# Performance work log

Hardware: AMD Instinct MI355X
Metric: run time of the kernel (lower is better)

The kernel has to match this reference:

```python
import jax, jax.numpy as jnp
import numpy as np

B, S, HID = 1, 2048, 4096
N_HEADS, N_KV_HEADS = 32, 8
HEAD_DIM = HID // N_HEADS  # 128


def setup_inputs() -> dict:
    key = jax.random.key(0)
    ks = jax.random.split(key, 5)
    w = 0.02  # init scale for weights
    return {
        "hidden_states": jax.random.normal(ks[0], (B, S, HID), dtype=jnp.float32),
        "Wq": jax.random.normal(ks[1], (HID, HID), dtype=jnp.float32) * w,
        "Wk": jax.random.normal(ks[2], (N_KV_HEADS * HEAD_DIM, HID), dtype=jnp.float32) * w,
        "Wv": jax.random.normal(ks[3], (N_KV_HEADS * HEAD_DIM, HID), dtype=jnp.float32) * w,
        "Wo": jax.random.normal(ks[4], (HID, HID), dtype=jnp.float32) * w,
        "n_init": 4,
        "n_local": 1024,
    }


def reference(hidden_states, Wq, Wk, Wv, Wo, n_init, n_local):
    b, s, hid = hidden_states.shape
    n_rep = N_HEADS // N_KV_HEADS
    scale = 1.0 / np.sqrt(HEAD_DIM).astype(np.float32)

    # QKV projections (torch Linear: y = x @ W.T)
    q = (hidden_states @ Wq.T).reshape(b, s, N_HEADS, HEAD_DIM).transpose(0, 2, 1, 3)
    k = (hidden_states @ Wk.T).reshape(b, s, N_KV_HEADS, HEAD_DIM).transpose(0, 2, 1, 3)
    v = (hidden_states @ Wv.T).reshape(b, s, N_KV_HEADS, HEAD_DIM).transpose(0, 2, 1, 3)

    # GQA: repeat KV heads to match query heads
    k = jnp.repeat(k, n_rep, axis=1)  # [b, H, s, d]
    v = jnp.repeat(v, n_rep, axis=1)

    scores = jnp.einsum('bhqd,bhkd->bhqk', q, k) * scale  # [b, H, s, s]

    # StreamingLLM mask: causal AND (attention sink OR sliding window)
    i = jnp.arange(s)[:, None]
    j = jnp.arange(s)[None, :]
    allowed = (j <= i) & ((j < n_init) | (i - j < n_local))  # [s, s]
    neg = jnp.finfo(scores.dtype).min
    scores = jnp.where(allowed[None, None], scores, neg)

    probs = jax.nn.softmax(scores, axis=-1)
    attn = jnp.einsum('bhqk,bhkd->bhqd', probs, v)  # [b, H, s, d]
    attn = attn.transpose(0, 2, 1, 3).reshape(b, s, hid)
    return attn @ Wo.T
```

## Files before the change

kernel.cpp:

```cpp
#include <hip/hip_runtime.h>
#include <hip/hip_bf16.h>

#define S     2048
#define HID   4096
#define NH    32
#define NKV   8
#define DH    128
#define KVD   1024
#define NQK   6144
#define KDIM  4096

typedef unsigned short ushort_t;
typedef __attribute__((ext_vector_type(8))) __bf16 bf16x8;
typedef __attribute__((ext_vector_type(8))) unsigned short u16x8;
typedef __attribute__((ext_vector_type(4))) float f32x4;

static __device__ __forceinline__ unsigned short f2b(float f) {
    union { float f; unsigned int i; } x; x.f = f;
    unsigned int r = (x.i + 0x7fffu + ((x.i >> 16) & 1u)) >> 16;
    return (unsigned short)r;
}

static __device__ __forceinline__ void gload16(const void* g, void* l) {
    __builtin_amdgcn_global_load_lds(
        (const __attribute__((address_space(1))) void*)g,
        (__attribute__((address_space(3))) void*)l, 16, 0, 0);
}

__global__ __launch_bounds__(256)
void cvt_f2b(const float* __restrict__ src, ushort_t* __restrict__ dst, int n4) {
    int i = blockIdx.x * 256 + threadIdx.x;
    if (i < n4) {
        float4 v = ((const float4*)src)[i];
        ushort4 o;
        o.x = f2b(v.x); o.y = f2b(v.y); o.z = f2b(v.z); o.w = f2b(v.w);
        ((ushort4*)dst)[i] = o;
    }
}

#define G_BM 256
#define G_BN 128
#define G_BK 64
#define BUF_USH ((G_BM + G_BN) * G_BK)
#define BOFF_B  (G_BM * G_BK)

#define STG_A(bb, kt2, j) gload16(gA[j] + (size_t)(kt2) * G_BK, &sm[(bb) + ldA[j]])
#define STG_B(bb, kt2, j) gload16(gB[j] + (size_t)(kt2) * G_BK, &sm[(bb) + ldB[j]])

template <int MODE>
__global__ __launch_bounds__(512, 2)
void gemm256(const ushort_t* __restrict__ A, const ushort_t* __restrict__ B,
             float* __restrict__ Cf, ushort_t* __restrict__ Qb,
             ushort_t* __restrict__ Kb, ushort_t* __restrict__ Vt,
             int M, int N, int K) {
    __shared__ __align__(16) ushort_t sm[3 * BUF_USH];

    const int tid   = threadIdx.x;
    const int w     = tid >> 6;
    const int lane  = tid & 63;
    const int mlane = lane & 15;
    const int q4    = lane >> 4;
    const int wr    = w >> 1, wc = w & 1;
    const int m0    = blockIdx.y * G_BM;
    const int n0    = blockIdx.x * G_BN;

    const ushort_t* gA[4];
    const ushort_t* gB[2];
    int ldA[4], ldB[2];
#pragma unroll
    for (int j = 0; j < 4; j++) {
        int c = j * 512 + tid, row = c >> 3, sl = (c & 7) ^ (row & 7);
        gA[j]  = A + (size_t)(m0 + row) * K + sl * 8;
        ldA[j] = (j * 512 + w * 64) * 8;
    }
#pragma unroll
    for (int j = 0; j < 2; j++) {
        int c = j * 512 + tid, row = c >> 3, sl = (c & 7) ^ (row & 7);
        gB[j]  = B + (size_t)(n0 + row) * K + sl * 8;
        ldB[j] = BOFF_B + (j * 512 + w * 64) * 8;
    }

    int offA[4][2], offB[4][2];
#pragma unroll
    for (int f = 0; f < 4; f++)
#pragma unroll
        for (int ks = 0; ks < 2; ks++) {
            int ra = wr * 64 + f * 16 + mlane;
            offA[f][ks] = ra * 64 + (((ks * 4 + q4) ^ (ra & 7)) * 8);
            int rb = wc * 64 + f * 16 + mlane;
            offB[f][ks] = BOFF_B + rb * 64 + (((ks * 4 + q4) ^ (rb & 7)) * 8);
        }

    f32x4 acc[4][4];
#pragma unroll
    for (int i = 0; i < 4; i++)
#pragma unroll
        for (int j = 0; j < 4; j++) acc[i][j] = (f32x4)(0.0f);

    const int NT = K / G_BK;

    STG_A(0, 0, 0); STG_A(0, 0, 1); STG_A(0, 0, 2); STG_A(0, 0, 3);
    STG_B(0, 0, 0); STG_B(0, 0, 1);
    STG_A(BUF_USH, 1, 0); STG_A(BUF_USH, 1, 1);
    STG_A(BUF_USH, 1, 2); STG_A(BUF_USH, 1, 3);
    STG_B(BUF_USH, 1, 0); STG_B(BUF_USH, 1, 1);
    asm volatile("s_waitcnt vmcnt(6)" ::: "memory");
    __builtin_amdgcn_s_barrier();

    int s_cur = 0;
    for (int kt = 0; kt < NT; kt++) {
        const int s_n2 = (s_cur >= 1) ? s_cur - 1 : 2;
        const int base = s_cur * BUF_USH;
        const int b2   = s_n2 * BUF_USH;
        const bool stg = (kt + 2) < NT;

#pragma unroll
        for (int p = 0; p < 4; p++) {
            const int qm = p >> 1, qn = p & 1;
            bf16x8 af[2][2], bq[2][2];
#pragma unroll
            for (int mi = 0; mi < 2; mi++)
#pragma unroll
                for (int ks = 0; ks < 2; ks++)
                    af[mi][ks] = *(const bf16x8*)&sm[base + offA[qm * 2 + mi][ks]];
#pragma unroll
            for (int ni = 0; ni < 2; ni++)
#pragma unroll
                for (int ks = 0; ks < 2; ks++)
                    bq[ni][ks] = *(const bf16x8*)&sm[base + offB[qn * 2 + ni][ks]];

            if (stg) {
                if (p == 0) { STG_A(b2, kt + 2, 0); STG_A(b2, kt + 2, 1); }
                if (p == 1) { STG_A(b2, kt + 2, 2); STG_A(b2, kt + 2, 3); }
                if (p == 2) { STG_B(b2, kt + 2, 0); }
                if (p == 3) { STG_B(b2, kt + 2, 1); }
            }

            __builtin_amdgcn_s_barrier();
            asm volatile("s_waitcnt lgkmcnt(0)");
            __builtin_amdgcn_s_setprio(1);
#pragma unroll
            for (int mi = 0; mi < 2; mi++)
#pragma unroll
                for (int ni = 0; ni < 2; ni++)
#pragma unroll
                    for (int ks = 0; ks < 2; ks++)
                        acc[qm * 2 + mi][qn * 2 + ni] =
                            __builtin_amdgcn_mfma_f32_16x16x32_bf16(
                                af[mi][ks], bq[ni][ks],
                                acc[qm * 2 + mi][qn * 2 + ni], 0, 0, 0);
            __builtin_amdgcn_s_setprio(0);
            __builtin_amdgcn_s_barrier();
        }

        if (stg) asm volatile("s_waitcnt vmcnt(6)" ::: "memory");
        else     asm volatile("s_waitcnt vmcnt(0)" ::: "memory");
        __builtin_amdgcn_s_barrier();
        s_cur = (s_cur == 2) ? 0 : s_cur + 1;
    }

#pragma unroll
    for (int fm = 0; fm < 4; fm++) {
#pragma unroll
        for (int fn = 0; fn < 4; fn++) {
            const int row = m0 + wr * 64 + fm * 16 + q4 * 4;
            const int col = n0 + wc * 64 + fn * 16 + mlane;
            if (MODE == 0) {
#pragma unroll
                for (int r = 0; r < 4; r++)
                    Cf[(size_t)(row + r) * N + col] = acc[fm][fn][r];
            } else {
                if (n0 < HID) {
#pragma unroll
                    for (int r = 0; r < 4; r++)
                        Qb[(size_t)(row + r) * HID + col] = f2b(acc[fm][fn][r]);
                } else if (n0 < HID + KVD) {
                    int c2 = col - HID;
#pragma unroll
                    for (int r = 0; r < 4; r++)
                        Kb[(size_t)(row + r) * KVD + c2] = f2b(acc[fm][fn][r]);
                } else {
                    int c2 = col - (HID + KVD);
                    ushort4 o;
                    o.x = f2b(acc[fm][fn][0]); o.y = f2b(acc[fm][fn][1]);
                    o.z = f2b(acc[fm][fn][2]); o.w = f2b(acc[fm][fn][3]);
                    *(ushort4*)(Vt + (size_t)c2 * S + row) = o;
                }
            }
        }
    }
}

__global__ __launch_bounds__(256)
void attn_mfma(const ushort_t* __restrict__ Qb, const ushort_t* __restrict__ Kb,
               const ushort_t* __restrict__ Vt, ushort_t* __restrict__ O,
               const int* __restrict__ n_init_p, const int* __restrict__ n_local_p) {
    __shared__ ushort_t Ks[4][32][40];
    __shared__ ushort_t Vs[128][40];
    __shared__ ushort_t Ps[4][16][40];

    const int n_init = *n_init_p, n_local = *n_local_p;
    const int tid   = threadIdx.x;
    const int w     = tid >> 6;
    const int lane  = tid & 63;
    const int mlane = lane & 15;
    const int q4    = lane >> 4;
    const int h     = blockIdx.x >> 5;
    const int qt    = blockIdx.x & 31;
    const int kh    = h >> 2;
    const int i0    = qt * 64;
    const int iMax  = i0 + 63;
    const int qrow_base = i0 + w * 16;

    bf16x8 qf[4];
    {
        const ushort_t* qp = Qb + (size_t)(qrow_base + mlane) * HID + h * DH + q4 * 8;
#pragma unroll
        for (int ks = 0; ks < 4; ks++) qf[ks] = *(const bf16x8*)(qp + ks * 32);
    }

    f32x4 oacc[8];
#pragma unroll
    for (int i = 0; i < 8; i++) oacc[i] = (f32x4)(0.0f);
    float lrow[4];
#pragma unroll
    for (int r = 0; r < 4; r++) lrow[r] = 0.0f;

    int wstart = i0 - n_local + 1; if (wstart < 0) wstart = 0;
    const int tw   = (wstart <= n_init) ? 0 : (wstart >> 5);
    const int tmax = iMax >> 5;
    const float scale = 0.08838834764831845f;

    const int skk = tid >> 4, sc = tid & 15;
    const int vd  = tid >> 2, vc = tid & 3;
    ushort_t* psw = &Ps[w][0][0];

    for (int t = 0; t <= tmax; t++) {
        if (t > 0 && t < tw) continue;
        const int j0 = t * 32;

        u16x8 ka = *(const u16x8*)(Kb + (size_t)(j0 + skk) * KVD + kh * DH + sc * 8);
        u16x8 kc = *(const u16x8*)(Kb + (size_t)(j0 + skk + 16) * KVD + kh * DH + sc * 8);
        u16x8 va = *(const u16x8*)(Vt + (size_t)(kh * DH + vd) * S + j0 + vc * 8);
        u16x8 vb = *(const u16x8*)(Vt + (size_t)(kh * DH + vd + 64) * S + j0 + vc * 8);
        __syncthreads();
        *(u16x8*)&Ks[sc >> 2][skk][(sc & 3) * 8] = ka;
        *(u16x8*)&Ks[sc >> 2][skk + 16][(sc & 3) * 8] = kc;
        *(u16x8*)&Vs[vd][vc * 8] = va;
        *(u16x8*)&Vs[vd + 64][vc * 8] = vb;
        __syncthreads();

        f32x4 sacc0 = (f32x4)(0.0f), sacc1 = (f32x4)(0.0f);
#pragma unroll
        for (int ks = 0; ks < 4; ks++) {
            bf16x8 k0f = *(const bf16x8*)&Ks[ks][mlane][q4 * 8];
            bf16x8 k1f = *(const bf16x8*)&Ks[ks][16 + mlane][q4 * 8];
            sacc0 = __builtin_amdgcn_mfma_f32_16x16x32_bf16(qf[ks], k0f, sacc0, 0, 0, 0);
            sacc1 = __builtin_amdgcn_mfma_f32_16x16x32_bf16(qf[ks], k1f, sacc1, 0, 0, 0);
        }

        const bool interior = (j0 + 31 <= i0) && (iMax - j0 < n_local);

#pragma unroll
        for (int r = 0; r < 4; r++) {
            float p0, p1;
            if (interior) {
                p0 = __expf(sacc0[r] * scale);
                p1 = __expf(sacc1[r] * scale);
            } else {
                int qi = qrow_base + q4 * 4 + r;
                int jA = j0 + mlane, jB = jA + 16;
                bool okA = (jA <= qi) && ((jA < n_init) || (qi - jA < n_local));
                bool okB = (jB <= qi) && ((jB < n_init) || (qi - jB < n_local));
                p0 = okA ? __expf(sacc0[r] * scale) : 0.0f;
                p1 = okB ? __expf(sacc1[r] * scale) : 0.0f;
            }
            lrow[r] += p0 + p1;
            psw[(q4 * 4 + r) * 40 + mlane]      = f2b(p0);
            psw[(q4 * 4 + r) * 40 + 16 + mlane] = f2b(p1);
        }

        bf16x8 pf = *(const bf16x8*)&psw[mlane * 40 + q4 * 8];
#pragma unroll
        for (int dt = 0; dt < 8; dt++) {
            bf16x8 vf = *(const bf16x8*)&Vs[dt * 16 + mlane][q4 * 8];
            oacc[dt] = __builtin_amdgcn_mfma_f32_16x16x32_bf16(pf, vf, oacc[dt], 0, 0, 0);
        }
    }

#pragma unroll
    for (int r = 0; r < 4; r++) {
#pragma unroll
        for (int off = 1; off < 16; off <<= 1)
            lrow[r] += __shfl_xor(lrow[r], off);
    }

#pragma unroll
    for (int r = 0; r < 4; r++) {
        float inv = 1.0f / lrow[r];
        int qrow = qrow_base + q4 * 4 + r;
        ushort_t* op = O + (size_t)qrow * HID + h * DH + mlane;
#pragma unroll
        for (int dt = 0; dt < 8; dt++)
            op[dt * 16] = f2b(oacc[dt][r] * inv);
    }
}

extern "C" void kernel_launch(void* const* d_in, const int* in_sizes, int n_in,
                              void* d_out, int out_size, void* d_ws, size_t ws_size,
                              hipStream_t stream) {
    const float* H  = (const float*)d_in[0];
    const float* Wq = (const float*)d_in[1];
    const float* Wk = (const float*)d_in[2];
    const float* Wv = (const float*)d_in[3];
    const float* Wo = (const float*)d_in[4];
    const int* n_init_p  = (const int*)d_in[5];
    const int* n_local_p = (const int*)d_in[6];

    char* p = (char*)d_ws;
    ushort_t* Hb   = (ushort_t*)p;  p += (size_t)S * HID * 2;
    ushort_t* Wbuf = (ushort_t*)p;  p += (size_t)NQK * KDIM * 2;
    ushort_t* Qb   = (ushort_t*)p;  p += (size_t)S * HID * 2;
    ushort_t* Kb   = (ushort_t*)p;  p += (size_t)S * KVD * 2;
    ushort_t* Vt   = (ushort_t*)p;
    ushort_t* Ab   = Hb;

    dim3 blk(256);
    const int nH = S * HID / 4, nWq = HID * KDIM / 4, nWk = KVD * KDIM / 4;

    cvt_f2b<<<dim3((nH  + 255) / 256), blk, 0, stream>>>(H,  Hb, nH);
    cvt_f2b<<<dim3((nWq + 255) / 256), blk, 0, stream>>>(Wq, Wbuf, nWq);
    cvt_f2b<<<dim3((nWk + 255) / 256), blk, 0, stream>>>(Wk, Wbuf + (size_t)HID * KDIM, nWk);
    cvt_f2b<<<dim3((nWk + 255) / 256), blk, 0, stream>>>(Wv, Wbuf + (size_t)(HID + KVD) * KDIM, nWk);
    gemm256<1><<<dim3(NQK / G_BN, S / G_BM), dim3(512), 0, stream>>>(
        Hb, Wbuf, nullptr, Qb, Kb, Vt, S, NQK, KDIM);
    attn_mfma<<<dim3(NH * (S / 64)), blk, 0, stream>>>(Qb, Kb, Vt, Ab, n_init_p, n_local_p);
    cvt_f2b<<<dim3((nWq + 255) / 256), blk, 0, stream>>>(Wo, Wbuf, nWq);
    gemm256<0><<<dim3(HID / G_BN, S / G_BM), dim3(512), 0, stream>>>(
        Ab, Wbuf, (float*)d_out, nullptr, nullptr, nullptr, S, HID, KDIM);
}
```

Before: 527.2 us.

## Split GEMM inner loop by k-slice instead of output quadrant for fragment reuse

```diff
diff --git a/kernel.cpp b/kernel.cpp
--- a/kernel.cpp
+++ b/kernel.cpp
@@ -115,40 +115,31 @@
         const bool stg = (kt + 2) < NT;
 
 #pragma unroll
-        for (int p = 0; p < 4; p++) {
-            const int qm = p >> 1, qn = p & 1;
-            bf16x8 af[2][2], bq[2][2];
-#pragma unroll
-            for (int mi = 0; mi < 2; mi++)
-#pragma unroll
-                for (int ks = 0; ks < 2; ks++)
-                    af[mi][ks] = *(const bf16x8*)&sm[base + offA[qm * 2 + mi][ks]];
-#pragma unroll
-            for (int ni = 0; ni < 2; ni++)
-#pragma unroll
-                for (int ks = 0; ks < 2; ks++)
-                    bq[ni][ks] = *(const bf16x8*)&sm[base + offB[qn * 2 + ni][ks]];
+        for (int p = 0; p < 2; p++) {
+            bf16x8 af2[4], bq2[4];
+#pragma unroll
+            for (int f = 0; f < 4; f++)
+                af2[f] = *(const bf16x8*)&sm[base + offA[f][p]];
+#pragma unroll
+            for (int f = 0; f < 4; f++)
+                bq2[f] = *(const bf16x8*)&sm[base + offB[f][p]];
 
             if (stg) {
-                if (p == 0) { STG_A(b2, kt + 2, 0); STG_A(b2, kt + 2, 1); }
-                if (p == 1) { STG_A(b2, kt + 2, 2); STG_A(b2, kt + 2, 3); }
-                if (p == 2) { STG_B(b2, kt + 2, 0); }
-                if (p == 3) { STG_B(b2, kt + 2, 1); }
+                if (p == 0) { STG_A(b2, kt + 2, 0); STG_A(b2, kt + 2, 1);
+                              STG_B(b2, kt + 2, 0); }
+                else        { STG_A(b2, kt + 2, 2); STG_A(b2, kt + 2, 3);
+                              STG_B(b2, kt + 2, 1); }
             }
 
             __builtin_amdgcn_s_barrier();
             asm volatile("s_waitcnt lgkmcnt(0)");
             __builtin_amdgcn_s_setprio(1);
 #pragma unroll
-            for (int mi = 0; mi < 2; mi++)
-#pragma unroll
-                for (int ni = 0; ni < 2; ni++)
-#pragma unroll
-                    for (int ks = 0; ks < 2; ks++)
-                        acc[qm * 2 + mi][qn * 2 + ni] =
-                            __builtin_amdgcn_mfma_f32_16x16x32_bf16(
-                                af[mi][ks], bq[ni][ks],
-                                acc[qm * 2 + mi][qn * 2 + ni], 0, 0, 0);
+            for (int mt = 0; mt < 4; mt++)
+#pragma unroll
+                for (int nt = 0; nt < 4; nt++)
+                    acc[mt][nt] = __builtin_amdgcn_mfma_f32_16x16x32_bf16(
+                        af2[mt], bq2[nt], acc[mt][nt], 0, 0, 0);
             __builtin_amdgcn_s_setprio(0);
             __builtin_amdgcn_s_barrier();
         }
```

Result: faster. 475.2 us (-9.9%).
